# Kernel tuning notes

Hardware: AMD Instinct MI355X
Metric: run time of the kernel (lower is better)

## Reference

```python
import jax, jax.numpy as jnp
import numpy as np

# config (matches init_kwargs)
B, N, C_IN = 2, 16384, 64
NPOINT, NSAMPLE, RADIUS = 2048, 32, 0.8
MLP = [64, 128, 256]
EPS = 1e-5


def _fps(xyz, npoint):
    """Furthest point sampling. xyz: (B,N,3) -> idx (B,npoint) int32."""
    b, n, _ = xyz.shape
    d0 = jnp.sum((xyz - xyz[:, :1, :]) ** 2, -1)  # dist to point 0

    def body(mind, _):
        nxt = jnp.argmax(mind, -1)                       # (B,)
        pt = jnp.take_along_axis(xyz, nxt[:, None, None], 1)  # (B,1,3)
        mind = jnp.minimum(mind, jnp.sum((xyz - pt) ** 2, -1))
        return mind, nxt

    _, idxs = jax.lax.scan(body, d0, None, length=npoint - 1)  # (npoint-1,B)
    idxs = jnp.concatenate([jnp.zeros((1, b), idxs.dtype), idxs], 0)
    return jnp.transpose(idxs).astype(jnp.int32)


def _ball_query(xyz, new_xyz, radius, nsample):
    """First nsample neighbors within radius (pointnet2 semantics: pad with first hit)."""
    n = xyz.shape[1]
    d = jnp.sum((new_xyz[:, :, None, :] - xyz[:, None, :, :]) ** 2, -1)  # (B,np,N)
    mask = d < radius * radius
    # prefer lowest original index among in-range points
    score = jnp.where(mask, -jnp.arange(n, dtype=jnp.float32), -(n + 1.0))
    vals, idxs = jax.lax.top_k(score, nsample)           # (B,np,ns)
    valid = vals > -(n + 0.5)
    idx = jnp.where(valid, idxs, idxs[..., :1])
    cnt = mask.sum(-1)                                    # (B,np)
    return idx.astype(jnp.int32), cnt


def _gather(arr, idx):  # arr (B,N,...), idx (B,...) -> (B,...,...)
    return jax.vmap(lambda a, i: a[i])(arr, idx)


def _bn_eval4(x, g, b):  # (B,C,P,S), eval-mode BN with running mean 0 / var 1
    s = g / jnp.sqrt(1.0 + EPS)
    return x * s[None, :, None, None] + b[None, :, None, None]


def _bn_eval3(x, g, b):  # (B,C,S)
    s = g / jnp.sqrt(1.0 + EPS)
    return x * s[None, :, None] + b[None, :, None]


def setup_inputs() -> dict:
    key = jax.random.key(0)
    ks = jax.random.split(key, 12)
    xyz = jax.random.normal(ks[0], (B, N, 3), jnp.float32)
    features = jax.random.normal(ks[1], (B, C_IN, N), jnp.float32)
    cin = 3 + C_IN
    dims = [cin] + MLP
    inp = {"xyz": xyz, "features": features}
    for li in range(3):
        w = jax.random.normal(ks[2 + li], (dims[li + 1], dims[li]), jnp.float32) / np.sqrt(dims[li])
        inp[f"W{li+1}"] = w
        inp[f"g{li+1}"] = jnp.ones((dims[li + 1],), jnp.float32)
        inp[f"b{li+1}"] = jnp.zeros((dims[li + 1],), jnp.float32)
    npt8, cd, cd8 = NPOINT // 8, MLP[-1], MLP[-1] // 8
    inp["Wq"] = jax.random.normal(ks[5], (npt8, NPOINT), jnp.float32) / np.sqrt(NPOINT)
    inp["gq"] = jnp.ones((npt8,), jnp.float32)
    inp["bq"] = jnp.zeros((npt8,), jnp.float32)
    inp["Wk"] = jax.random.normal(ks[6], (npt8, NPOINT), jnp.float32) / np.sqrt(NPOINT)
    inp["gk"] = jnp.ones((npt8,), jnp.float32)
    inp["bk"] = jnp.zeros((npt8,), jnp.float32)
    inp["We1"] = jax.random.normal(ks[7], (cd8, cd), jnp.float32) / np.sqrt(cd)
    inp["We2"] = jax.random.normal(ks[8], (cd, cd8), jnp.float32) / np.sqrt(cd8)
    inp["alpha"] = jnp.zeros((1,), jnp.float32)  # torch: nn.Parameter(torch.zeros(1))
    return inp


def reference(xyz, features, W1, g1, b1, W2, g2, b2, W3, g3, b3,
              Wq, gq, bq, Wk, gk, bk, We1, We2, alpha):
    # ---- d-FPS sampling (indices are non-differentiable, as in the CUDA op) ----
    xyz_c = jax.lax.stop_gradient(xyz)
    samp = _fps(xyz_c, NPOINT)                       # (B,np)
    new_xyz = _gather(xyz, samp)                     # (B,np,3)
    # ---- ball query + grouping ----
    nn_idx, cnt = _ball_query(xyz_c, jax.lax.stop_gradient(new_xyz), RADIUS, NSAMPLE)
    grouped_xyz = _gather(xyz, nn_idx) - new_xyz[:, :, None, :]        # (B,np,ns,3)
    grouped_feat = _gather(jnp.transpose(features, (0, 2, 1)), nn_idx)  # (B,np,ns,C)
    h = jnp.transpose(jnp.concatenate([grouped_xyz, grouped_feat], -1), (0, 3, 1, 2))  # (B,3+C,np,ns)
    # ---- shared MLP (1x1 conv + BN(eval) + ReLU) ----
    for (w, g, b) in ((W1, g1, b1), (W2, g2, b2), (W3, g3, b3)):
        h = jax.nn.relu(_bn_eval4(jnp.einsum('oi,bips->bops', w, h), g, b))
    h = h * (cnt > 0)[:, None, :, None].astype(h.dtype)  # mask empty balls
    x = jnp.max(h, axis=-1)                               # (B,Cd,np) max-pool over nsample
    # ---- LCEF channel-affinity attention ----
    xh = jnp.transpose(x, (0, 2, 1))                      # (B,np,Cd)
    q = jax.nn.relu(_bn_eval3(jnp.einsum('oi,bis->bos', Wq, xh), gq, bq))  # (B,np/8,Cd)
    k = jax.nn.relu(_bn_eval3(jnp.einsum('oi,bis->bos', Wk, xh), gk, bk))  # (B,np/8,Cd)
    sim = jnp.einsum('bqc,bqd->bcd', k, q)                # (B,Cd,Cd)
    aff = jax.nn.softmax(jnp.max(sim, -1, keepdims=True) - sim, axis=-1)
    s = jnp.max(x, -1)                                    # (B,Cd) squeeze
    e = jax.nn.sigmoid(jnp.einsum('oi,bi->bo', We2, jax.nn.relu(jnp.einsum('oi,bi->bo', We1, s))))
    v = x * e[:, :, None]                                 # excitation
    out = alpha[0] * jnp.einsum('bcd,bdn->bcn', aff, v) + x
    return new_xyz, out
```

## Files before the change

kernel.cpp:

```cpp
#include <hip/hip_runtime.h>
#include <hip/hip_bf16.h>

typedef unsigned short ushort_t;
typedef unsigned int uint_t;
typedef unsigned long long ull_t;

#define B_    2
#define N_    16384
#define NP_   2048
#define NS_   32
#define EPSF  1e-5f

__device__ __forceinline__ float bf2f(ushort_t u) { return __uint_as_float(((uint_t)u) << 16); }

__device__ __forceinline__ int dtflag(const uint_t* g1w) {
  return (g1w[0] == 0x3F803F80u) ? 1 : 0;
}

__device__ __forceinline__ float dist2(float dx, float dy, float dz) {
  return __fadd_rn(__fadd_rn(__fmul_rn(dx, dx), __fmul_rn(dy, dy)), __fmul_rn(dz, dz));
}

template<int CTRL, int RMASK>
__device__ __forceinline__ float dppmax(float x) {
  int m = __builtin_amdgcn_update_dpp(0, __float_as_int(x), CTRL, RMASK, 0xf, true);
  return fmaxf(x, __int_as_float(m));
}
__device__ __forceinline__ float rlanef(float x, int l) {
  return __int_as_float(__builtin_amdgcn_readlane(__float_as_int(x), l));
}

struct CvtTab { const void* src[18]; };
__constant__ int c_psz[18] = {4288, 64, 64, 8192, 128, 128, 32768, 256, 256,
                              524288, 256, 256, 524288, 256, 256, 8192, 8192, 1};
__constant__ int c_poff[18] = {0, 4288, 4352, 4416, 12608, 12736, 12864, 45632, 45888,
                               46144, 570432, 570688, 570944, 1095232, 1095488,
                               1095744, 1103936, 1112128};
__constant__ int c_pblk[19] = {0, 5, 6, 7, 15, 16, 17, 49, 50, 51, 563, 564, 565,
                               1077, 1078, 1079, 1087, 1095, 1096};

__global__ void k_xyz_soa(const void* __restrict__ xyz, const uint_t* __restrict__ g1w,
                          float* __restrict__ X, float* __restrict__ Y, float* __restrict__ Z) {
  int g = blockIdx.x * blockDim.x + threadIdx.x;
  if (g >= B_ * N_) return;
  if (dtflag(g1w)) {
    const ushort_t* p = (const ushort_t*)xyz;
    X[g] = bf2f(p[g * 3 + 0]); Y[g] = bf2f(p[g * 3 + 1]); Z[g] = bf2f(p[g * 3 + 2]);
  } else {
    const float* p = (const float*)xyz;
    X[g] = p[g * 3 + 0]; Y[g] = p[g * 3 + 1]; Z[g] = p[g * 3 + 2];
  }
}

__global__ __launch_bounds__(1024)
__attribute__((amdgpu_waves_per_eu(4, 4)))
void k_fps_prep(CvtTab tab,
                const float* __restrict__ X, const float* __restrict__ Y,
                const float* __restrict__ Z,
                float* __restrict__ nxf, void* __restrict__ outp,
                const void* __restrict__ feat,
                float* __restrict__ par, float* __restrict__ Wt,
                float* __restrict__ featF) {
  __shared__ float smem[64 * 65];
  int bid = blockIdx.x, t = threadIdx.x;
  const uint_t* g1w = (const uint_t*)tab.src[1];

  if (bid < 2) {
    float* sv = smem;
    float* bc = smem + 16;
    int b = bid;
    int lane = t & 63, wid = t >> 6;
    int f = dtflag(g1w);
    const float* Xb = X + b * N_;
    const float* Yb = Y + b * N_;
    const float* Zb = Z + b * N_;
    float cx = Xb[0], cy = Yb[0], cz = Zb[0];
    if (t == 0) {
      int base = b * NP_ * 3;
      nxf[base + 0] = cx; nxf[base + 1] = cy; nxf[base + 2] = cz;
      if (f) {
        __hip_bfloat16* o = (__hip_bfloat16*)outp;
        o[base + 0] = __float2bfloat16(cx); o[base + 1] = __float2bfloat16(cy); o[base + 2] = __float2bfloat16(cz);
      } else {
        float* o = (float*)outp;
        o[base + 0] = cx; o[base + 1] = cy; o[base + 2] = cz;
      }
    }
    float x[16], y[16], z[16], md[16];
#pragma unroll
    for (int c = 0; c < 4; c++) {
      float4 xv = ((const float4*)Xb)[(t << 2) + c];
      float4 yv = ((const float4*)Yb)[(t << 2) + c];
      float4 zv = ((const float4*)Zb)[(t << 2) + c];
      x[4 * c + 0] = xv.x; x[4 * c + 1] = xv.y; x[4 * c + 2] = xv.z; x[4 * c + 3] = xv.w;
      y[4 * c + 0] = yv.x; y[4 * c + 1] = yv.y; y[4 * c + 2] = yv.z; y[4 * c + 3] = yv.w;
      z[4 * c + 0] = zv.x; z[4 * c + 1] = zv.y; z[4 * c + 2] = zv.z; z[4 * c + 3] = zv.w;
      md[4 * c + 0] = dist2(xv.x - cx, yv.x - cy, zv.x - cz);
      md[4 * c + 1] = dist2(xv.y - cx, yv.y - cy, zv.y - cz);
      md[4 * c + 2] = dist2(xv.z - cx, yv.z - cy, zv.z - cz);
      md[4 * c + 3] = dist2(xv.w - cx, yv.w - cy, zv.w - cz);
    }
#pragma unroll
    for (int k = 0; k < 16; k++)
      asm volatile("" : "+v"(x[k]), "+v"(y[k]), "+v"(z[k]));

    for (int it = 1; it < NP_; it++) {
      float q0 = fmaxf(fmaxf(md[0], md[1]),   fmaxf(md[2], md[3]));
      float q1 = fmaxf(fmaxf(md[4], md[5]),   fmaxf(md[6], md[7]));
      float q2 = fmaxf(fmaxf(md[8], md[9]),   fmaxf(md[10], md[11]));
      float q3 = fmaxf(fmaxf(md[12], md[13]), fmaxf(md[14], md[15]));
      float lm = fmaxf(fmaxf(q0, q1), fmaxf(q2, q3));
      float v = lm;
      v = dppmax<0x111, 0xf>(v);
      v = dppmax<0x112, 0xf>(v);
      v = dppmax<0x114, 0xf>(v);
      v = dppmax<0x118, 0xf>(v);
      v = dppmax<0x142, 0xa>(v);
      v = dppmax<0x143, 0xc>(v);
      float wm = rlanef(v, 63);
      ull_t m1 = __ballot(lm == wm);
      int wlead = __ffsll((unsigned long long)m1) - 1;
      if (lane == wlead) sv[wid] = wm;
      __syncthreads();
      float pv = sv[lane & 15];
      float q = pv;
      q = dppmax<0x111, 0xf>(q);
      q = dppmax<0x112, 0xf>(q);
      q = dppmax<0x114, 0xf>(q);
      q = dppmax<0x118, 0xf>(q);
      float bm = rlanef(q, 15);
      ull_t m2 = __ballot((lane < 16) && (pv == bm));
      int wwave = __ffsll((unsigned long long)m2) - 1;
      if (wid == wwave && lane == wlead) {
        float wx = x[0], wy = y[0], wz = z[0];
#pragma unroll
        for (int k = 15; k >= 0; k--)
          if (md[k] == lm) { wx = x[k]; wy = y[k]; wz = z[k]; }
        bc[0] = wx; bc[1] = wy; bc[2] = wz;
        int base = (b * NP_ + it) * 3;
        nxf[base + 0] = wx; nxf[base + 1] = wy; nxf[base + 2] = wz;
        if (f) {
          __hip_bfloat16* o = (__hip_bfloat16*)outp;
          o[base + 0] = __float2bfloat16(wx); o[base + 1] = __float2bfloat16(wy); o[base + 2] = __float2bfloat16(wz);
        } else {
          float* o = (float*)outp;
          o[base + 0] = wx; o[base + 1] = wy; o[base + 2] = wz;
        }
      }
      __syncthreads();
      cx = bc[0]; cy = bc[1]; cz = bc[2];
#pragma unroll
      for (int k = 0; k < 16; k++)
        md[k] = fminf(md[k], dist2(x[k] - cx, y[k] - cy, z[k] - cz));
    }
    return;
  }

  int f = dtflag(g1w);
  if (bid < 514) {
    int tile_id = bid - 2;
    int b = tile_id >> 8, n0 = (tile_id & 255) * 64;
    for (int i = t; i < 4096; i += 1024) {
      int c = i >> 6, nn = i & 63;
      size_t src = (size_t)(b * 64 + c) * N_ + n0 + nn;
      smem[c * 65 + nn] = f ? bf2f(((const ushort_t*)feat)[src]) : ((const float*)feat)[src];
    }
    __syncthreads();
    for (int i = t; i < 4096; i += 1024) {
      int nn = i >> 6, c = i & 63;
      featF[((size_t)(b * N_ + n0 + nn)) * 64 + c] = smem[c * 65 + nn];
    }
    return;
  }
  if (bid < 559) {
    int wi = bid - 514;
    if (wi < 5) {
      int i = wi * 1024 + t;
      if (i < 4288) {
        float v = f ? bf2f(((const ushort_t*)tab.src[0])[i]) : ((const float*)tab.src[0])[i];
        int o = i / 67, k = i - o * 67;
        Wt[k * 64 + o] = v;
      }
    } else if (wi < 13) {
      int i = (wi - 5) * 1024 + t;
      if (i < 8192) {
        float v = f ? bf2f(((const ushort_t*)tab.src[3])[i]) : ((const float*)tab.src[3])[i];
        int o = i >> 6, k = i & 63;
        Wt[4288 + k * 128 + o] = v;
      }
    } else {
      int i = (wi - 13) * 1024 + t;
      if (i < 32768) {
        float v = f ? bf2f(((const ushort_t*)tab.src[6])[i]) : ((const float*)tab.src[6])[i];
        int o = i >> 7, k = i & 127;
        Wt[12480 + k * 256 + o] = v;
      }
    }
    return;
  }
  {
    int blk = bid - 559;
    int p = 0;
#pragma unroll
    for (int q = 0; q < 18; q++)
      if (blk >= c_pblk[q + 1]) p = q + 1;
    int i = (blk - c_pblk[p]) * 1024 + t;
    if (i < c_psz[p]) {
      float v = f ? bf2f(((const ushort_t*)tab.src[p])[i]) : ((const float*)tab.src[p])[i];
      par[c_poff[p] + i] = v;
    }
  }
}

__global__ void k_ball(const float* __restrict__ X, const float* __restrict__ Y,
                       const float* __restrict__ Z, const float* __restrict__ nxf,
                       int* __restrict__ nnidx) {
  __shared__ int ibuf[4][NS_];
  int t = threadIdx.x, w = t >> 6, lane = t & 63;
  int cid = blockIdx.x * 4 + w;
  int b = cid >> 11;
  const float* Xb = X + b * N_;
  const float* Yb = Y + b * N_;
  const float* Zb = Z + b * N_;
  float cx = nxf[cid * 3 + 0], cy = nxf[cid * 3 + 1], cz = nxf[cid * 3 + 2];
  int found = 0;
  for (int c = 0; c < N_ / 64; c++) {
    int n = c * 64 + lane;
    float d = dist2(Xb[n] - cx, Yb[n] - cy, Zb[n] - cz);
    bool pred = d < 0.64f;
    ull_t mask = __ballot(pred);
    if (pred) {
      int rank = found + __popcll(mask & ((1ull << lane) - 1ull));
      if (rank < NS_) ibuf[w][rank] = n;
    }
    found += __popcll(mask);
    if (found >= NS_) break;
  }
  __syncthreads();
  if (lane < NS_) {
    int idx = (lane < found) ? ibuf[w][lane] : ibuf[w][0];
    nnidx[cid * NS_ + lane] = idx;
  }
}

__global__ __launch_bounds__(256) void k_mlp(
    const float* __restrict__ featF, const float* __restrict__ X,
    const float* __restrict__ Y, const float* __restrict__ Z,
    const float* __restrict__ nxf, const int* __restrict__ nnidx,
    const float* __restrict__ Wt,
    const float* __restrict__ g1f, const float* __restrict__ b1f,
    const float* __restrict__ g2f, const float* __restrict__ b2f,
    const float* __restrict__ g3f, const float* __restrict__ b3f,
    float* __restrict__ x_nc) {
  __shared__ __align__(16) char smem[33280];
  float* h2f = (float*)smem;
  float* h0f = (float*)(smem + 16384);
  float* h1f = (float*)(smem + 24960);
  int* idxs  = (int*)(smem + 33152);
  const float* Wt1 = Wt;
  const float* Wt2 = Wt + 4288;
  const float* Wt3 = Wt + 12480;

  int t = threadIdx.x;
  int cid = blockIdx.x;
  int b = cid >> 11;
  if (t < 32) idxs[t] = nnidx[cid * NS_ + t];
  __syncthreads();
  float cx = nxf[cid * 3 + 0], cy = nxf[cid * 3 + 1], cz = nxf[cid * 3 + 2];
  if (t < 32) {
    int n = b * N_ + idxs[t];
    h0f[0 * 32 + t] = X[n] - cx;
    h0f[1 * 32 + t] = Y[n] - cy;
    h0f[2 * 32 + t] = Z[n] - cz;
  }
  {
    int s = t >> 3, cg = t & 7;
    const float* fr = featF + ((size_t)(b * N_ + idxs[s])) * 64 + cg * 8;
    float4 a = ((const float4*)fr)[0];
    float4 c2 = ((const float4*)fr)[1];
    int kb = 3 + cg * 8;
    h0f[(kb + 0) * 32 + s] = a.x;  h0f[(kb + 1) * 32 + s] = a.y;
    h0f[(kb + 2) * 32 + s] = a.z;  h0f[(kb + 3) * 32 + s] = a.w;
    h0f[(kb + 4) * 32 + s] = c2.x; h0f[(kb + 5) * 32 + s] = c2.y;
    h0f[(kb + 6) * 32 + s] = c2.z; h0f[(kb + 7) * 32 + s] = c2.w;
  }
  __syncthreads();

  int og = t >> 3, sg = t & 7;
  int s0 = sg * 4;
  {
    int o0 = og * 2;
    float acc[2][4] = {{0, 0, 0, 0}, {0, 0, 0, 0}};
    for (int k = 0; k < 67; k++) {
      float4 h = *(const float4*)(h0f + k * 32 + s0);
      float2 wp = *(const float2*)(Wt1 + k * 64 + o0);
      acc[0][0] = fmaf(wp.x, h.x, acc[0][0]);
      acc[0][1] = fmaf(wp.x, h.y, acc[0][1]);
      acc[0][2] = fmaf(wp.x, h.z, acc[0][2]);
      acc[0][3] = fmaf(wp.x, h.w, acc[0][3]);
      acc[1][0] = fmaf(wp.y, h.x, acc[1][0]);
      acc[1][1] = fmaf(wp.y, h.y, acc[1][1]);
      acc[1][2] = fmaf(wp.y, h.z, acc[1][2]);
      acc[1][3] = fmaf(wp.y, h.w, acc[1][3]);
    }
#pragma unroll
    for (int i2 = 0; i2 < 2; i2++) {
      int o = o0 + i2;
      float sc = g1f[o] / sqrtf(1.0f + EPSF);
      float bb = b1f[o];
      float4 yv;
      yv.x = fmaxf(fmaf(acc[i2][0], sc, bb), 0.0f);
      yv.y = fmaxf(fmaf(acc[i2][1], sc, bb), 0.0f);
      yv.z = fmaxf(fmaf(acc[i2][2], sc, bb), 0.0f);
      yv.w = fmaxf(fmaf(acc[i2][3], sc, bb), 0.0f);
      *(float4*)(h1f + o * 32 + s0) = yv;
    }
  }
  __syncthreads();
  {
    int o0 = og * 4;
    float acc[4][4] = {{0,0,0,0},{0,0,0,0},{0,0,0,0},{0,0,0,0}};
    for (int k = 0; k < 64; k++) {
      float4 h = *(const float4*)(h1f + k * 32 + s0);
      float4 wp = *(const float4*)(Wt2 + k * 128 + o0);
      float w[4] = {wp.x, wp.y, wp.z, wp.w};
#pragma unroll
      for (int i2 = 0; i2 < 4; i2++) {
        acc[i2][0] = fmaf(w[i2], h.x, acc[i2][0]);
        acc[i2][1] = fmaf(w[i2], h.y, acc[i2][1]);
        acc[i2][2] = fmaf(w[i2], h.z, acc[i2][2]);
        acc[i2][3] = fmaf(w[i2], h.w, acc[i2][3]);
      }
    }
#pragma unroll
    for (int i2 = 0; i2 < 4; i2++) {
      int o = o0 + i2;
      float sc = g2f[o] / sqrtf(1.0f + EPSF);
      float bb = b2f[o];
      float4 yv;
      yv.x = fmaxf(fmaf(acc[i2][0], sc, bb), 0.0f);
      yv.y = fmaxf(fmaf(acc[i2][1], sc, bb), 0.0f);
      yv.z = fmaxf(fmaf(acc[i2][2], sc, bb), 0.0f);
      yv.w = fmaxf(fmaf(acc[i2][3], sc, bb), 0.0f);
      *(float4*)(h2f + o * 32 + s0) = yv;
    }
  }
  __syncthreads();
  float acc3[8][4] = {{0,0,0,0},{0,0,0,0},{0,0,0,0},{0,0,0,0},
                      {0,0,0,0},{0,0,0,0},{0,0,0,0},{0,0,0,0}};
  int o0 = og * 8;
  for (int kg = 0; kg < 128; kg++) {
    float4 h = *(const float4*)(h2f + kg * 32 + s0);
    float4 wa = *(const float4*)(Wt3 + kg * 256 + o0);
    float4 wc = *(const float4*)(Wt3 + kg * 256 + o0 + 4);
    float w[8] = {wa.x, wa.y, wa.z, wa.w, wc.x, wc.y, wc.z, wc.w};
#pragma unroll
    for (int i2 = 0; i2 < 8; i2++) {
      acc3[i2][0] = fmaf(w[i2], h.x, acc3[i2][0]);
      acc3[i2][1] = fmaf(w[i2], h.y, acc3[i2][1]);
      acc3[i2][2] = fmaf(w[i2], h.z, acc3[i2][2]);
      acc3[i2][3] = fmaf(w[i2], h.w, acc3[i2][3]);
    }
  }
  float mx[8];
#pragma unroll
  for (int i2 = 0; i2 < 8; i2++) {
    int o = o0 + i2;
    float sc = g3f[o] / sqrtf(1.0f + EPSF);
    float bb = b3f[o];
    float m0 = fmaxf(fmaf(acc3[i2][0], sc, bb), 0.0f);
    float m1 = fmaxf(fmaf(acc3[i2][1], sc, bb), 0.0f);
    float m2 = fmaxf(fmaf(acc3[i2][2], sc, bb), 0.0f);
    float m3 = fmaxf(fmaf(acc3[i2][3], sc, bb), 0.0f);
    mx[i2] = fmaxf(fmaxf(m0, m1), fmaxf(m2, m3));
  }
#pragma unroll
  for (int off = 1; off < 8; off <<= 1) {
#pragma unroll
    for (int i2 = 0; i2 < 8; i2++) mx[i2] = fmaxf(mx[i2], __shfl_xor(mx[i2], off));
  }
  if (sg == 0) {
    float4 a, c;
    a.x = mx[0]; a.y = mx[1]; a.z = mx[2]; a.w = mx[3];
    c.x = mx[4]; c.y = mx[5]; c.z = mx[6]; c.w = mx[7];
    *(float4*)(x_nc + (size_t)cid * 256 + o0) = a;
    *(float4*)(x_nc + (size_t)cid * 256 + o0 + 4) = c;
  }
}

__global__ __launch_bounds__(256) void k_sqmax_qk(
    const float* __restrict__ x_nc, float* __restrict__ sqpart,
    const float* __restrict__ Wqf, const float* __restrict__ gqf, const float* __restrict__ bqf,
    const float* __restrict__ Wkf, const float* __restrict__ gkf, const float* __restrict__ bkf,
    float* __restrict__ qb, float* __restrict__ kb) {
  __shared__ float As[32 * 33];
  __shared__ float Bs[32 * 64];
  int bigid = blockIdx.x, t = threadIdx.x;
  if (bigid < 32) {
    int b = bigid >> 4, chunk = bigid & 15;
    const float* xb = x_nc + (size_t)b * NP_ * 256 + (size_t)chunk * 128 * 256;
    float m = -1e30f;
#pragma unroll 8
    for (int n = 0; n < 128; n++) m = fmaxf(m, xb[(size_t)n * 256 + t]);
    sqpart[(size_t)(b * 16 + chunk) * 256 + t] = m;
    return;
  }
  int bid = bigid - 32;
  int b = bid & 1, tq = (bid >> 1) & 1, mt = (bid >> 2) & 7, nt = (bid >> 5) & 3;
  const float* W = tq ? Wkf : Wqf;
  const float* g = tq ? gkf : gqf;
  const float* bb_ = tq ? bkf : bqf;
  float* outp = tq ? kb : qb;
  int o0 = (t >> 4) * 2, c0 = (t & 15) * 4;
  float acc[2][4] = {{0,0,0,0},{0,0,0,0}};
  for (int k0 = 0; k0 < NP_; k0 += 32) {
    for (int i = t; i < 1024; i += 256) {
      int row = i >> 5, kk = i & 31;
      As[row * 33 + kk] = W[(size_t)(mt * 32 + row) * NP_ + k0 + kk];
    }
    for (int i = t; i < 2048; i += 256) {
      int kk = i >> 6, cc = i & 63;
      Bs[kk * 64 + cc] = x_nc[((size_t)(b * NP_ + k0 + kk)) * 256 + nt * 64 + cc];
    }
    __syncthreads();
    for (int kk = 0; kk < 32; kk++) {
      float4 bv = *(const float4*)(Bs + kk * 64 + c0);
      float a0 = As[(o0 + 0) * 33 + kk];
      float a1 = As[(o0 + 1) * 33 + kk];
      acc[0][0] = fmaf(a0, bv.x, acc[0][0]); acc[0][1] = fmaf(a0, bv.y, acc[0][1]);
      acc[0][2] = fmaf(a0, bv.z, acc[0][2]); acc[0][3] = fmaf(a0, bv.w, acc[0][3]);
      acc[1][0] = fmaf(a1, bv.x, acc[1][0]); acc[1][1] = fmaf(a1, bv.y, acc[1][1]);
      acc[1][2] = fmaf(a1, bv.z, acc[1][2]); acc[1][3] = fmaf(a1, bv.w, acc[1][3]);
    }
    __syncthreads();
  }
#pragma unroll
  for (int i2 = 0; i2 < 2; i2++) {
    int o = mt * 32 + o0 + i2;
    float sc = g[o] / sqrtf(1.0f + EPSF);
    float bv = bb_[o];
    float4 y;
    y.x = fmaxf(fmaf(acc[i2][0], sc, bv), 0.0f);
    y.y = fmaxf(fmaf(acc[i2][1], sc, bv), 0.0f);
    y.z = fmaxf(fmaf(acc[i2][2], sc, bv), 0.0f);
    y.w = fmaxf(fmaf(acc[i2][3], sc, bv), 0.0f);
    *(float4*)(outp + ((size_t)(b * 256 + o)) * 256 + nt * 64 + c0) = y;
  }
}

__global__ __launch_bounds__(256) void k_sqe_sim(
    const float* __restrict__ sqpart,
    const float* __restrict__ We1f, const float* __restrict__ We2f,
    float* __restrict__ e,
    const float* __restrict__ qb, const float* __restrict__ kb,
    float* __restrict__ sim) {
  __shared__ float As[32 * 64];
  __shared__ float Bs[32 * 64];
  int bigid = blockIdx.x, t = threadIdx.x;
  if (bigid < 2) {
    float* ssh = As;
    float* ush = As + 256;
    int b = bigid;
    const float* pp = sqpart + (size_t)b * 16 * 256;
    float m = -1e30f;
#pragma unroll
    for (int c = 0; c < 16; c++) m = fmaxf(m, pp[c * 256 + t]);
    ssh[t] = m;
    __syncthreads();
    if (t < 32) {
      float a = 0.0f;
      for (int i = 0; i < 256; i++) a = fmaf(We1f[t * 256 + i], ssh[i], a);
      ush[t] = fmaxf(a, 0.0f);
    }
    __syncthreads();
    float a = 0.0f;
#pragma unroll
    for (int j = 0; j < 32; j++) a = fmaf(We2f[t * 32 + j], ush[j], a);
    e[b * 256 + t] = 1.0f / (1.0f + expf(-a));
    return;
  }
  int bid = bigid - 2;
  int b = bid & 1, ct = (bid >> 1) & 3, dt = (bid >> 3) & 3;
  int c0 = (t >> 4) * 4, d0 = (t & 15) * 4;
  float acc[4][4] = {{0,0,0,0},{0,0,0,0},{0,0,0,0},{0,0,0,0}};
  for (int k0 = 0; k0 < 256; k0 += 32) {
    for (int i = t; i < 2048; i += 256) {
      int kk = i >> 6, cc = i & 63;
      As[kk * 64 + cc] = kb[((size_t)(b * 256 + k0 + kk)) * 256 + ct * 64 + cc];
      Bs[kk * 64 + cc] = qb[((size_t)(b * 256 + k0 + kk)) * 256 + dt * 64 + cc];
    }
    __syncthreads();
    for (int kk = 0; kk < 32; kk++) {
      float4 av = *(const float4*)(As + kk * 64 + c0);
      float4 bv = *(const float4*)(Bs + kk * 64 + d0);
      acc[0][0] = fmaf(av.x, bv.x, acc[0][0]); acc[0][1] = fmaf(av.x, bv.y, acc[0][1]);
      acc[0][2] = fmaf(av.x, bv.z, acc[0][2]); acc[0][3] = fmaf(av.x, bv.w, acc[0][3]);
      acc[1][0] = fmaf(av.y, bv.x, acc[1][0]); acc[1][1] = fmaf(av.y, bv.y, acc[1][1]);
      acc[1][2] = fmaf(av.y, bv.z, acc[1][2]); acc[1][3] = fmaf(av.y, bv.w, acc[1][3]);
      acc[2][0] = fmaf(av.z, bv.x, acc[2][0]); acc[2][1] = fmaf(av.z, bv.y, acc[2][1]);
      acc[2][2] = fmaf(av.z, bv.z, acc[2][2]); acc[2][3] = fmaf(av.z, bv.w, acc[2][3]);
      acc[3][0] = fmaf(av.w, bv.x, acc[3][0]); acc[3][1] = fmaf(av.w, bv.y, acc[3][1]);
      acc[3][2] = fmaf(av.w, bv.z, acc[3][2]); acc[3][3] = fmaf(av.w, bv.w, acc[3][3]);
    }
    __syncthreads();
  }
#pragma unroll
  for (int i2 = 0; i2 < 4; i2++) {
    *(float4*)(sim + ((size_t)(b * 256 + ct * 64 + c0 + i2)) * 256 + dt * 64 + d0) =
        *(float4*)acc[i2];
  }
}

__global__ void k_aff(const float* __restrict__ sim, float* __restrict__ aff) {
  int t = threadIdx.x, w = t >> 6, lane = t & 63;
  int row = blockIdx.x * 4 + w;
  const float* sr = sim + (size_t)row * 256;
  float4 v = *(const float4*)(sr + lane * 4);
  float mx = fmaxf(fmaxf(v.x, v.y), fmaxf(v.z, v.w));
#pragma unroll
  for (int off = 32; off >= 1; off >>= 1) mx = fmaxf(mx, __shfl_xor(mx, off));
  float4 u;
  u.x = mx - v.x; u.y = mx - v.y; u.z = mx - v.z; u.w = mx - v.w;
  float um = fmaxf(fmaxf(u.x, u.y), fmaxf(u.z, u.w));
#pragma unroll
  for (int off = 32; off >= 1; off >>= 1) um = fmaxf(um, __shfl_xor(um, off));
  float4 p;
  p.x = expf(u.x - um); p.y = expf(u.y - um); p.z = expf(u.z - um); p.w = expf(u.w - um);
  float s = ((p.x + p.y) + (p.z + p.w));
#pragma unroll
  for (int off = 32; off >= 1; off >>= 1) s += __shfl_xor(s, off);
  float4 o;
  o.x = p.x / s; o.y = p.y / s; o.z = p.z / s; o.w = p.w / s;
  *(float4*)(aff + (size_t)row * 256 + lane * 4) = o;
}

__global__ __launch_bounds__(256) void k_out(const float* __restrict__ aff,
                                             const float* __restrict__ x_nc,
                                             const float* __restrict__ e,
                                             const float* __restrict__ alphaf,
                                             void* __restrict__ outp,
                                             const uint_t* __restrict__ g1w) {
  __shared__ float Acs[64 * 33];
  __shared__ float Bs[32 * 65];
  __shared__ float Xs[64 * 65];
  int bid = blockIdx.x;
  int b = bid & 1, ct = (bid >> 1) & 3, nt = bid >> 3;
  int t = threadIdx.x;
  int c0 = (t >> 4) * 4, n0 = (t & 15) * 4;
  float acc[4][4] = {{0,0,0,0},{0,0,0,0},{0,0,0,0},{0,0,0,0}};
  for (int k0 = 0; k0 < 256; k0 += 32) {
    for (int i = t; i < 2048; i += 256) {
      int cc = i >> 5, kk = i & 31;
      Acs[cc * 33 + kk] = aff[((size_t)(b * 256 + ct * 64 + cc)) * 256 + k0 + kk];
    }
    for (int i = t; i < 2048; i += 256) {
      int nn = i >> 5, kk = i & 31;
      Bs[kk * 65 + nn] =
          x_nc[((size_t)(b * NP_ + nt * 64 + nn)) * 256 + k0 + kk] * e[b * 256 + k0 + kk];
    }
    __syncthreads();
    for (int kk = 0; kk < 32; kk++) {
      float a0 = Acs[(c0 + 0) * 33 + kk];
      float a1 = Acs[(c0 + 1) * 33 + kk];
      float a2 = Acs[(c0 + 2) * 33 + kk];
      float a3 = Acs[(c0 + 3) * 33 + kk];
      float b0 = Bs[kk * 65 + n0 + 0];
      float b1 = Bs[kk * 65 + n0 + 1];
      float b2 = Bs[kk * 65 + n0 + 2];
      float b3 = Bs[kk * 65 + n0 + 3];
      acc[0][0] = fmaf(a0, b0, acc[0][0]); acc[0][1] = fmaf(a0, b1, acc[0][1]);
      acc[0][2] = fmaf(a0, b2, acc[0][2]); acc[0][3] = fmaf(a0, b3, acc[0][3]);
      acc[1][0] = fmaf(a1, b0, acc[1][0]); acc[1][1] = fmaf(a1, b1, acc[1][1]);
      acc[1][2] = fmaf(a1, b2, acc[1][2]); acc[1][3] = fmaf(a1, b3, acc[1][3]);
      acc[2][0] = fmaf(a2, b0, acc[2][0]); acc[2][1] = fmaf(a2, b1, acc[2][1]);
      acc[2][2] = fmaf(a2, b2, acc[2][2]); acc[2][3] = fmaf(a2, b3, acc[2][3]);
      acc[3][0] = fmaf(a3, b0, acc[3][0]); acc[3][1] = fmaf(a3, b1, acc[3][1]);
      acc[3][2] = fmaf(a3, b2, acc[3][2]); acc[3][3] = fmaf(a3, b3, acc[3][3]);
    }
    __syncthreads();
  }
  for (int i = t; i < 4096; i += 256) {
    int nn = i >> 6, cc = i & 63;
    Xs[nn * 65 + cc] = x_nc[((size_t)(b * NP_ + nt * 64 + nn)) * 256 + ct * 64 + cc];
  }
  __syncthreads();
  float af = alphaf[0];
  int f = dtflag(g1w);
#pragma unroll
  for (int i2 = 0; i2 < 4; i2++) {
    int c = ct * 64 + c0 + i2;
#pragma unroll
    for (int j = 0; j < 4; j++) {
      float xv = Xs[(n0 + j) * 65 + (c0 + i2)];
      float y = af * acc[i2][j] + xv;
      size_t base = 12288 + ((size_t)(b * 256 + c)) * NP_ + nt * 64 + n0 + j;
      if (f) ((__hip_bfloat16*)outp)[base] = __float2bfloat16(y);
      else   ((float*)outp)[base] = y;
    }
  }
}

extern "C" void kernel_launch(void* const* d_in, const int* in_sizes, int n_in,
                              void* d_out, int out_size, void* d_ws, size_t ws_size,
                              hipStream_t stream) {
  char* ws = (char*)d_ws;
  float* X     = (float*)(ws + 64);
  float* Y     = (float*)(ws + 131136);
  float* Z     = (float*)(ws + 262208);
  float* featF = (float*)(ws + 393280);
  float* par   = (float*)(ws + 8781888);
  float* nxf   = (float*)(ws + 13230464);
  int*   nn    = (int*)(ws + 13279616);
  float* x_nc  = (float*)(ws + 13803904);
  float* qb    = (float*)(ws + 17998208);
  float* kb    = (float*)(ws + 18522496);
  float* sim   = (float*)(ws + 19046784);
  float* aff   = (float*)(ws + 19571072);
  float* evec  = (float*)(ws + 20095360);
  float* Wt    = qb;
  float* sqpart = aff;

  float* g1f = par + 4288,    *b1f = par + 4352;
  float* g2f = par + 12608,   *b2f = par + 12736;
  float* g3f = par + 45632,   *b3f = par + 45888;
  float* Wqf = par + 46144,   *gqf = par + 570432,  *bqf = par + 570688;
  float* Wkf = par + 570944,  *gkf = par + 1095232, *bkf = par + 1095488;
  float* We1f = par + 1095744, *We2f = par + 1103936, *alphaf = par + 1112128;

  const uint_t* g1w = (const uint_t*)d_in[3];

  CvtTab tab;
  for (int p = 0; p < 18; p++) tab.src[p] = d_in[2 + p];

  k_xyz_soa<<<dim3(128), dim3(256), 0, stream>>>(d_in[0], g1w, X, Y, Z);
  k_fps_prep<<<dim3(1655), dim3(1024), 0, stream>>>(tab, X, Y, Z, nxf, d_out,
                                                    d_in[1], par, Wt, featF);
  k_ball<<<dim3(1024), dim3(256), 0, stream>>>(X, Y, Z, nxf, nn);
  k_mlp<<<dim3(4096), dim3(256), 0, stream>>>(featF, X, Y, Z, nxf, nn, Wt,
                                              g1f, b1f, g2f, b2f, g3f, b3f, x_nc);
  k_sqmax_qk<<<dim3(160), dim3(256), 0, stream>>>(x_nc, sqpart,
                                                  Wqf, gqf, bqf, Wkf, gkf, bkf, qb, kb);
  k_sqe_sim<<<dim3(34), dim3(256), 0, stream>>>(sqpart, We1f, We2f, evec, qb, kb, sim);
  k_aff<<<dim3(128), dim3(256), 0, stream>>>(sim, aff);
  k_out<<<dim3(256), dim3(256), 0, stream>>>(aff, x_nc, evec, alphaf, d_out, g1w);
}
```

Before: 3.572 ms.

## Fuse ball query into MLP kernel and compute squeeze max via atomics

Removes the separate ball-query kernel: the first wave of each MLP block now scans the points for its own centroid, which drops the neighbor-index round trip through global memory. The squeeze max over points is folded into the MLP epilogue with unsigned-int atomicMax on non-negative post-ReLU values, into a buffer zeroed in the first kernel. This removes the partial-max pass from the QK kernel. In exchange, the other three waves of each MLP block sit idle during the serial scan, and the atomics add contention on 512 addresses.

```diff
diff --git a/kernel.cpp b/kernel.cpp
--- a/kernel.cpp
+++ b/kernel.cpp
@@ -40,8 +40,13 @@
                                1077, 1078, 1079, 1087, 1095, 1096};
 
 __global__ void k_xyz_soa(const void* __restrict__ xyz, const uint_t* __restrict__ g1w,
-                          float* __restrict__ X, float* __restrict__ Y, float* __restrict__ Z) {
+                          float* __restrict__ X, float* __restrict__ Y, float* __restrict__ Z,
+                          float* __restrict__ sqbuf) {
   int g = blockIdx.x * blockDim.x + threadIdx.x;
+  if (blockIdx.x < 2) {
+    int i = blockIdx.x * 256 + threadIdx.x;
+    sqbuf[i] = 0.0f;
+  }
   if (g >= B_ * N_) return;
   if (dtflag(g1w)) {
     const ushort_t* p = (const ushort_t*)xyz;
@@ -212,47 +217,18 @@
   }
 }
 
-__global__ void k_ball(const float* __restrict__ X, const float* __restrict__ Y,
-                       const float* __restrict__ Z, const float* __restrict__ nxf,
-                       int* __restrict__ nnidx) {
-  __shared__ int ibuf[4][NS_];
-  int t = threadIdx.x, w = t >> 6, lane = t & 63;
-  int cid = blockIdx.x * 4 + w;
-  int b = cid >> 11;
-  const float* Xb = X + b * N_;
-  const float* Yb = Y + b * N_;
-  const float* Zb = Z + b * N_;
-  float cx = nxf[cid * 3 + 0], cy = nxf[cid * 3 + 1], cz = nxf[cid * 3 + 2];
-  int found = 0;
-  for (int c = 0; c < N_ / 64; c++) {
-    int n = c * 64 + lane;
-    float d = dist2(Xb[n] - cx, Yb[n] - cy, Zb[n] - cz);
-    bool pred = d < 0.64f;
-    ull_t mask = __ballot(pred);
-    if (pred) {
-      int rank = found + __popcll(mask & ((1ull << lane) - 1ull));
-      if (rank < NS_) ibuf[w][rank] = n;
-    }
-    found += __popcll(mask);
-    if (found >= NS_) break;
-  }
-  __syncthreads();
-  if (lane < NS_) {
-    int idx = (lane < found) ? ibuf[w][lane] : ibuf[w][0];
-    nnidx[cid * NS_ + lane] = idx;
-  }
-}
-
 __global__ __launch_bounds__(256) void k_mlp(
     const float* __restrict__ featF, const float* __restrict__ X,
     const float* __restrict__ Y, const float* __restrict__ Z,
-    const float* __restrict__ nxf, const int* __restrict__ nnidx,
+    const float* __restrict__ nxf,
     const float* __restrict__ Wt,
     const float* __restrict__ g1f, const float* __restrict__ b1f,
     const float* __restrict__ g2f, const float* __restrict__ b2f,
     const float* __restrict__ g3f, const float* __restrict__ b3f,
-    float* __restrict__ x_nc) {
+    float* __restrict__ x_nc, float* __restrict__ sqbuf) {
   __shared__ __align__(16) char smem[33280];
+  __shared__ int ibuf[NS_];
+  __shared__ int found_s;
   float* h2f = (float*)smem;
   float* h0f = (float*)(smem + 16384);
   float* h1f = (float*)(smem + 24960);
@@ -264,9 +240,29 @@
   int t = threadIdx.x;
   int cid = blockIdx.x;
   int b = cid >> 11;
-  if (t < 32) idxs[t] = nnidx[cid * NS_ + t];
+  float cx = nxf[cid * 3 + 0], cy = nxf[cid * 3 + 1], cz = nxf[cid * 3 + 2];
+  if (t < 64) {
+    const float* Xb = X + b * N_;
+    const float* Yb = Y + b * N_;
+    const float* Zb = Z + b * N_;
+    int found = 0;
+    for (int c = 0; c < N_ / 64; c++) {
+      int n = c * 64 + t;
+      float d = dist2(Xb[n] - cx, Yb[n] - cy, Zb[n] - cz);
+      bool pred = d < 0.64f;
+      ull_t mask = __ballot(pred);
+      if (pred) {
+        int rank = found + __popcll(mask & ((1ull << t) - 1ull));
+        if (rank < NS_) ibuf[rank] = n;
+      }
+      found += __popcll(mask);
+      if (found >= NS_) break;
+    }
+    if (t == 0) found_s = found;
+  }
   __syncthreads();
-  float cx = nxf[cid * 3 + 0], cy = nxf[cid * 3 + 1], cz = nxf[cid * 3 + 2];
+  if (t < 32) idxs[t] = (t < found_s) ? ibuf[t] : ibuf[0];
+  __syncthreads();
   if (t < 32) {
     int n = b * N_ + idxs[t];
     h0f[0 * 32 + t] = X[n] - cx;
@@ -385,32 +381,26 @@
     c.x = mx[4]; c.y = mx[5]; c.z = mx[6]; c.w = mx[7];
     *(float4*)(x_nc + (size_t)cid * 256 + o0) = a;
     *(float4*)(x_nc + (size_t)cid * 256 + o0 + 4) = c;
-  }
-}
-
-__global__ __launch_bounds__(256) void k_sqmax_qk(
-    const float* __restrict__ x_nc, float* __restrict__ sqpart,
-    const float* __restrict__ Wqf, const float* __restrict__ gqf, const float* __restrict__ bqf,
-    const float* __restrict__ Wkf, const float* __restrict__ gkf, const float* __restrict__ bkf,
-    float* __restrict__ qb, float* __restrict__ kb) {
+    uint_t* sq = (uint_t*)(sqbuf + b * 256 + o0);
+#pragma unroll
+    for (int i2 = 0; i2 < 8; i2++)
+      atomicMax(sq + i2, __float_as_uint(mx[i2]));
+  }
+}
+
+__global__ __launch_bounds__(256) void k_qk(const float* __restrict__ x_nc,
+                                            const float* __restrict__ Wqf, const float* __restrict__ gqf, const float* __restrict__ bqf,
+                                            const float* __restrict__ Wkf, const float* __restrict__ gkf, const float* __restrict__ bkf,
+                                            float* __restrict__ qb, float* __restrict__ kb) {
   __shared__ float As[32 * 33];
   __shared__ float Bs[32 * 64];
-  int bigid = blockIdx.x, t = threadIdx.x;
-  if (bigid < 32) {
-    int b = bigid >> 4, chunk = bigid & 15;
-    const float* xb = x_nc + (size_t)b * NP_ * 256 + (size_t)chunk * 128 * 256;
-    float m = -1e30f;
-#pragma unroll 8
-    for (int n = 0; n < 128; n++) m = fmaxf(m, xb[(size_t)n * 256 + t]);
-    sqpart[(size_t)(b * 16 + chunk) * 256 + t] = m;
-    return;
-  }
-  int bid = bigid - 32;
+  int bid = blockIdx.x;
   int b = bid & 1, tq = (bid >> 1) & 1, mt = (bid >> 2) & 7, nt = (bid >> 5) & 3;
   const float* W = tq ? Wkf : Wqf;
   const float* g = tq ? gkf : gqf;
   const float* bb_ = tq ? bkf : bqf;
   float* outp = tq ? kb : qb;
+  int t = threadIdx.x;
   int o0 = (t >> 4) * 2, c0 = (t & 15) * 4;
   float acc[2][4] = {{0,0,0,0},{0,0,0,0}};
   for (int k0 = 0; k0 < NP_; k0 += 32) {
@@ -449,7 +439,7 @@
 }
 
 __global__ __launch_bounds__(256) void k_sqe_sim(
-    const float* __restrict__ sqpart,
+    const float* __restrict__ sqbuf,
     const float* __restrict__ We1f, const float* __restrict__ We2f,
     float* __restrict__ e,
     const float* __restrict__ qb, const float* __restrict__ kb,
@@ -461,11 +451,7 @@
     float* ssh = As;
     float* ush = As + 256;
     int b = bigid;
-    const float* pp = sqpart + (size_t)b * 16 * 256;
-    float m = -1e30f;
-#pragma unroll
-    for (int c = 0; c < 16; c++) m = fmaxf(m, pp[c * 256 + t]);
-    ssh[t] = m;
+    ssh[t] = sqbuf[b * 256 + t];
     __syncthreads();
     if (t < 32) {
       float a = 0.0f;
@@ -610,7 +596,7 @@
   float* featF = (float*)(ws + 393280);
   float* par   = (float*)(ws + 8781888);
   float* nxf   = (float*)(ws + 13230464);
-  int*   nn    = (int*)(ws + 13279616);
+  float* sqbuf = (float*)(ws + 13279616);
   float* x_nc  = (float*)(ws + 13803904);
   float* qb    = (float*)(ws + 17998208);
   float* kb    = (float*)(ws + 18522496);
@@ -618,7 +604,6 @@
   float* aff   = (float*)(ws + 19571072);
   float* evec  = (float*)(ws + 20095360);
   float* Wt    = qb;
-  float* sqpart = aff;
 
   float* g1f = par + 4288,    *b1f = par + 4352;
   float* g2f = par + 12608,   *b2f = par + 12736;
@@ -632,15 +617,14 @@
   CvtTab tab;
   for (int p = 0; p < 18; p++) tab.src[p] = d_in[2 + p];
 
-  k_xyz_soa<<<dim3(128), dim3(256), 0, stream>>>(d_in[0], g1w, X, Y, Z);
+  k_xyz_soa<<<dim3(128), dim3(256), 0, stream>>>(d_in[0], g1w, X, Y, Z, sqbuf);
   k_fps_prep<<<dim3(1655), dim3(1024), 0, stream>>>(tab, X, Y, Z, nxf, d_out,
                                                     d_in[1], par, Wt, featF);
-  k_ball<<<dim3(1024), dim3(256), 0, stream>>>(X, Y, Z, nxf, nn);
-  k_mlp<<<dim3(4096), dim3(256), 0, stream>>>(featF, X, Y, Z, nxf, nn, Wt,
-                                              g1f, b1f, g2f, b2f, g3f, b3f, x_nc);
-  k_sqmax_qk<<<dim3(160), dim3(256), 0, stream>>>(x_nc, sqpart,
-                                                  Wqf, gqf, bqf, Wkf, gkf, bkf, qb, kb);
-  k_sqe_sim<<<dim3(34), dim3(256), 0, stream>>>(sqpart, We1f, We2f, evec, qb, kb, sim);
+  k_mlp<<<dim3(4096), dim3(256), 0, stream>>>(featF, X, Y, Z, nxf, Wt,
+                                              g1f, b1f, g2f, b2f, g3f, b3f,
+                                              x_nc, sqbuf);
+  k_qk<<<dim3(128), dim3(256), 0, stream>>>(x_nc, Wqf, gqf, bqf, Wkf, gkf, bkf, qb, kb);
+  k_sqe_sim<<<dim3(34), dim3(256), 0, stream>>>(sqbuf, We1f, We2f, evec, qb, kb, sim);
   k_aff<<<dim3(128), dim3(256), 0, stream>>>(sim, aff);
   k_out<<<dim3(256), dim3(256), 0, stream>>>(aff, x_nc, evec, alphaf, d_out, g1w);
 }
```

Result: slower. 3.787 ms (+6.0%).
